# Kernel tuning notes

Hardware: AMD Instinct MI355X
Metric: run time of the kernel (lower is better)

Reference implementation:

```python
import jax, jax.numpy as jnp
import numpy as np

IN_DIM = 128
HID = 128
NUM_CLASSES = 10
N_NODES = 100000
N_EDGES = 1600000
NUM_GRAPHS = 128


def setup_inputs() -> dict:
    key = jax.random.key(0)
    ks = jax.random.split(key, 12)
    X = jax.random.normal(ks[0], (N_NODES, IN_DIM), dtype=jnp.float32)
    EI = jax.random.randint(ks[1], (2, N_EDGES), 0, N_NODES, dtype=jnp.int64)
    batch = jnp.sort(jax.random.randint(ks[2], (N_NODES,), 0, NUM_GRAPHS, dtype=jnp.int64))
    s_in = 1.0 / np.sqrt(IN_DIM)
    s_h = 1.0 / np.sqrt(HID)
    s_m = 1.0 / np.sqrt(2 * HID)
    params = {
        'W1': jax.random.uniform(ks[3], (IN_DIM, HID), jnp.float32, -s_in, s_in),
        'b1': jnp.zeros((HID,), jnp.float32),
        'W2': jax.random.uniform(ks[4], (HID, HID), jnp.float32, -s_h, s_h),
        'b2': jnp.zeros((HID,), jnp.float32),
        'W3': jax.random.uniform(ks[5], (HID, HID), jnp.float32, -s_h, s_h),
        'b3': jnp.zeros((HID,), jnp.float32),
        'Wm1': jax.random.uniform(ks[6], (2 * HID, HID), jnp.float32, -s_m, s_m),
        'bm1': jnp.zeros((HID,), jnp.float32),
        'Wm2': jax.random.uniform(ks[7], (HID, NUM_CLASSES), jnp.float32, -s_h, s_h),
        'bm2': jnp.zeros((NUM_CLASSES,), jnp.float32),
    }
    return dict(X=X, EI=EI, batch=batch, num_graphs=NUM_GRAPHS, **params)


def _gcn_norm(EI, n):
    # add self loops, compute D^{-1/2}[row] * D^{-1/2}[col]
    loops = jnp.arange(n, dtype=EI.dtype)
    row = jnp.concatenate([EI[0], loops])
    col = jnp.concatenate([EI[1], loops])
    deg = jax.ops.segment_sum(jnp.ones_like(row, dtype=jnp.float32), row, num_segments=n)
    dis = (deg + 1e-12) ** -0.5
    norm = dis[row] * dis[col]
    return row, col, norm


def _gcn_layer(x, row, col, norm, W, b):
    h = x @ W + b                       # [N, out]
    msg = h[col] * norm[:, None]        # gather + scale  [E+N, out]
    return jax.ops.segment_sum(msg, row, num_segments=x.shape[0])  # scatter-add


def _pool_mean_max(x, batch, num_graphs):
    s = jax.ops.segment_sum(x, batch, num_segments=num_graphs)
    cnt = jax.ops.segment_sum(jnp.ones((x.shape[0],), x.dtype), batch, num_segments=num_graphs)
    mean = s / (cnt[:, None] + 1e-12)
    mx = jax.ops.segment_max(x, batch, num_segments=num_graphs)
    return jnp.concatenate([mean, mx], axis=1)


def reference(X, EI, batch, num_graphs, W1, b1, W2, b2, W3, b3, Wm1, bm1, Wm2, bm2):
    n = X.shape[0]
    row, col, norm = _gcn_norm(EI, n)
    x = jax.nn.relu(_gcn_layer(X, row, col, norm, W1, b1))
    x = jax.nn.relu(_gcn_layer(x, row, col, norm, W2, b2))
    x = jax.nn.relu(_gcn_layer(x, row, col, norm, W3, b3))
    g = _pool_mean_max(x, batch, num_graphs)
    h = jax.nn.relu(g @ Wm1 + bm1)
    return h @ Wm2 + bm2
```

## Files before the change

kernel.cpp:

```cpp
#include <hip/hip_runtime.h>
#include <hip/hip_fp16.h>
#include <cstdint>
#include <cstddef>

#define DIM 128
#define NG 128
#define NCLS 10
#define PSLICE 8
#define CPAD 64
#define NXCD 8
#define NOWN 32
#define OPX (NOWN / NXCD)
#define NPBLK 1024
#define OCAP 112
#define GRAB 8
#define XCCID_IMM ((31 << 11) | (0 << 6) | 20)

typedef _Float16 f16;
typedef __attribute__((ext_vector_type(8))) _Float16 f16x8;
typedef __attribute__((ext_vector_type(4))) float f32x4;


__global__ __launch_bounds__(256) void k_part(
    const int* __restrict__ rw, const int* __restrict__ cl, int E, int N,
    unsigned long long* __restrict__ buckets, int* __restrict__ bcnt) {
  __shared__ int lcnt[NOWN];
  if (threadIdx.x < NOWN) lcnt[threadIdx.x] = 0;
  __syncthreads();
  int b = blockIdx.x;
  int C = (E + NPBLK - 1) / NPBLK;
  int s = b * C;
  int e = s + C;
  if (e > E) e = E;
  for (int i = s + (int)threadIdx.x; i < e; i += 256) {
    int r = rw[i], c = cl[i];
    int o = (int)(((long long)r * NOWN) / N);
    int sl = atomicAdd(&lcnt[o], 1);
    if (sl < OCAP)
      buckets[((size_t)o * NPBLK + b) * OCAP + sl] =
          ((unsigned long long)(unsigned)r << 32) | (unsigned)c;
  }
  __syncthreads();
  if (threadIdx.x < NOWN) {
    int v = lcnt[threadIdx.x];
    bcnt[threadIdx.x * NPBLK + b] = v < OCAP ? v : OCAP;
  }
}

__global__ __launch_bounds__(256) void k_place(
    const unsigned long long* __restrict__ buckets, const int* __restrict__ bcnt,
    int* __restrict__ cnt, int* __restrict__ csrc, int* __restrict__ work) {
  __shared__ int sg;
  const int ngrab = OPX * NPBLK / GRAB;
  unsigned xcc = __builtin_amdgcn_s_getreg(XCCID_IMM) & (NXCD - 1);
  for (;;) {
    if (threadIdx.x == 0) sg = atomicAdd(&work[xcc], 1);
    __syncthreads();
    int g = sg;
    __syncthreads();
    if (g >= ngrab) break;
    int owner = (int)xcc * OPX + g / (NPBLK / GRAB);
    int blk0 = (g % (NPBLK / GRAB)) * GRAB;
    const int* bc = bcnt + owner * NPBLK + blk0;
    const unsigned long long* bp =
        buckets + ((size_t)owner * NPBLK + blk0) * OCAP;
    for (int j = (int)threadIdx.x; j < GRAB * OCAP; j += 256) {
      int bb = j / OCAP;
      int pos = j % OCAP;
      if (pos < bc[bb]) {
        unsigned long long ent = bp[(size_t)bb * OCAP + pos];
        int r = (int)(unsigned)(ent >> 32);
        int c = (int)(unsigned)(ent & 0xffffffffu);
        int sl = atomicAdd(&cnt[r], 1);
        if (sl < CPAD) csrc[(r << 6) + sl] = c;
      }
    }
  }
}

__global__ void k_dis(const int* __restrict__ cnt, float* __restrict__ dis, int N) {
  int i = blockIdx.x * blockDim.x + threadIdx.x;
  if (i < N) {
    float d = (float)(cnt[i] + 1);
    dis[i] = 1.0f / sqrtf(d);
  }
}

__global__ void k_wt(const float* __restrict__ W1, const float* __restrict__ W2,
                     const float* __restrict__ W3, __half* __restrict__ Wt1,
                     __half* __restrict__ Wt2, __half* __restrict__ Wt3) {
  int gi = blockIdx.x * 256 + threadIdx.x;
  int m = gi / (DIM * DIM);
  int i = gi % (DIM * DIM);
  const float* W = (m == 0) ? W1 : (m == 1) ? W2 : W3;
  __half* Wt = (m == 0) ? Wt1 : (m == 1) ? Wt2 : Wt3;
  int k = i >> 7, c = i & 127;
  Wt[(size_t)c * DIM + k] = __float2half(W[(size_t)k * DIM + c]);
}


template <int FP32IN>
__global__ __launch_bounds__(256, 3) void k_gemm(
    const void* __restrict__ Ain, const __half* __restrict__ Wt,
    const float* __restrict__ bias, const float* __restrict__ dis,
    __half* __restrict__ Hh, int N) {
  int t = threadIdx.x;
  int lane = t & 63;
  int wv = t >> 6;
  int l15 = lane & 15, lg = lane >> 4;
  int cb = (wv & 1) * 64;

  f16x8 bfr[4][4];
#pragma unroll
  for (int ct = 0; ct < 4; ++ct) {
    int c = cb + ct * 16 + l15;
    const f16* wp = (const f16*)Wt + (size_t)c * DIM + lg * 8;
#pragma unroll
    for (int ks = 0; ks < 4; ++ks) bfr[ks][ct] = *(const f16x8*)(wp + ks * 32);
  }
  float bv[4];
#pragma unroll
  for (int ct = 0; ct < 4; ++ct) bv[ct] = bias[cb + ct * 16 + l15];

  const int nt2 = (N + 31) / 32;
  for (int t2 = blockIdx.x; t2 < nt2; t2 += gridDim.x) {
    int row0 = t2 * 32 + (wv >> 1) * 16;
    int rA = row0 + l15;
    if (rA > N - 1) rA = N - 1;
    f16x8 afr[4];
    if constexpr (FP32IN) {
      const float* ap = (const float*)Ain + (size_t)rA * DIM + lg * 8;
#pragma unroll
      for (int ks = 0; ks < 4; ++ks) {
        float4 v0 = *(const float4*)(ap + ks * 32);
        float4 v1 = *(const float4*)(ap + ks * 32 + 4);
        f16x8 a;
        a[0] = (f16)v0.x; a[1] = (f16)v0.y; a[2] = (f16)v0.z; a[3] = (f16)v0.w;
        a[4] = (f16)v1.x; a[5] = (f16)v1.y; a[6] = (f16)v1.z; a[7] = (f16)v1.w;
        afr[ks] = a;
      }
    } else {
      const f16* ap = (const f16*)Ain + (size_t)rA * DIM + lg * 8;
#pragma unroll
      for (int ks = 0; ks < 4; ++ks) afr[ks] = *(const f16x8*)(ap + ks * 32);
    }

    f32x4 acc[4];
#pragma unroll
    for (int ct = 0; ct < 4; ++ct) acc[ct] = (f32x4){0.f, 0.f, 0.f, 0.f};
#pragma unroll
    for (int ks = 0; ks < 4; ++ks)
#pragma unroll
      for (int ct = 0; ct < 4; ++ct)
        acc[ct] = __builtin_amdgcn_mfma_f32_16x16x32_f16(afr[ks], bfr[ks][ct], acc[ct], 0, 0, 0);

#pragma unroll
    for (int j = 0; j < 4; ++j) {
      int r = row0 + lg * 4 + j;
      if (r < N) {
        float dr = dis[r];
#pragma unroll
        for (int ct = 0; ct < 4; ++ct) {
          float o = (acc[ct][j] + bv[ct]) * dr;
          Hh[(size_t)r * DIM + cb + ct * 16 + l15] = __float2half(o);
        }
      }
    }
  }
}


__global__ __launch_bounds__(256) void k_agg(
    const __half* __restrict__ Hh, __half* __restrict__ Ah,
    const int* __restrict__ csrc, const int* __restrict__ cntA,
    const float* __restrict__ dis, int N) {
  int wid = (int)(((size_t)blockIdx.x * blockDim.x + threadIdx.x) >> 6);
  int lane = threadIdx.x & 63;
  if (wid >= N) return;
  int half = lane >> 5;
  int q = lane & 31;
  int cnt = cntA[wid];
  if (cnt > CPAD) cnt = CPAD;
  float dr = dis[wid];
  const int* cp = csrc + ((size_t)wid << 6);
  float4 a0 = {0.f, 0.f, 0.f, 0.f};
  float4 a1 = {0.f, 0.f, 0.f, 0.f};
  float4 a2 = {0.f, 0.f, 0.f, 0.f};
  float4 a3 = {0.f, 0.f, 0.f, 0.f};
  int i = half;
  for (; i + 6 < cnt; i += 8) {
    int c0 = cp[i], c1 = cp[i + 2], c2 = cp[i + 4], c3 = cp[i + 6];
    uint2 u0 = *(const uint2*)(Hh + (size_t)c0 * DIM + q * 4);
    uint2 u1 = *(const uint2*)(Hh + (size_t)c1 * DIM + q * 4);
    uint2 u2 = *(const uint2*)(Hh + (size_t)c2 * DIM + q * 4);
    uint2 u3 = *(const uint2*)(Hh + (size_t)c3 * DIM + q * 4);
    float2 f;
    f = __half22float2(*reinterpret_cast<__half2*>(&u0.x)); a0.x += f.x; a0.y += f.y;
    f = __half22float2(*reinterpret_cast<__half2*>(&u0.y)); a0.z += f.x; a0.w += f.y;
    f = __half22float2(*reinterpret_cast<__half2*>(&u1.x)); a1.x += f.x; a1.y += f.y;
    f = __half22float2(*reinterpret_cast<__half2*>(&u1.y)); a1.z += f.x; a1.w += f.y;
    f = __half22float2(*reinterpret_cast<__half2*>(&u2.x)); a2.x += f.x; a2.y += f.y;
    f = __half22float2(*reinterpret_cast<__half2*>(&u2.y)); a2.z += f.x; a2.w += f.y;
    f = __half22float2(*reinterpret_cast<__half2*>(&u3.x)); a3.x += f.x; a3.y += f.y;
    f = __half22float2(*reinterpret_cast<__half2*>(&u3.y)); a3.z += f.x; a3.w += f.y;
  }
  for (; i < cnt; i += 2) {
    int c0 = cp[i];
    uint2 u0 = *(const uint2*)(Hh + (size_t)c0 * DIM + q * 4);
    float2 f;
    f = __half22float2(*reinterpret_cast<__half2*>(&u0.x)); a0.x += f.x; a0.y += f.y;
    f = __half22float2(*reinterpret_cast<__half2*>(&u0.y)); a0.z += f.x; a0.w += f.y;
  }
  float ax = (a0.x + a1.x) + (a2.x + a3.x);
  float ay = (a0.y + a1.y) + (a2.y + a3.y);
  float az = (a0.z + a1.z) + (a2.z + a3.z);
  float aw = (a0.w + a1.w) + (a2.w + a3.w);
  ax += __shfl_xor(ax, 32);
  ay += __shfl_xor(ay, 32);
  az += __shfl_xor(az, 32);
  aw += __shfl_xor(aw, 32);
  if (lane < 32) {
    uint2 us = *(const uint2*)(Hh + (size_t)wid * DIM + q * 4);
    float2 s0 = __half22float2(*reinterpret_cast<__half2*>(&us.x));
    float2 s1 = __half22float2(*reinterpret_cast<__half2*>(&us.y));
    float ox = fmaxf(dr * (ax + s0.x), 0.f);
    float oy = fmaxf(dr * (ay + s0.y), 0.f);
    float oz = fmaxf(dr * (az + s1.x), 0.f);
    float ow = fmaxf(dr * (aw + s1.y), 0.f);
    __half2 p0 = __floats2half2_rn(ox, oy);
    __half2 p1 = __floats2half2_rn(oz, ow);
    uint2 u;
    u.x = *(unsigned int*)&p0;
    u.y = *(unsigned int*)&p1;
    *(uint2*)(Ah + (size_t)wid * DIM + q * 4) = u;
  }
}


__global__ void k_bounds(const int* __restrict__ batch, int N, int G,
                         int* __restrict__ starts) {
  int i = blockIdx.x * blockDim.x + threadIdx.x;
  if (i >= N) return;
  int b = batch[i];
  int pb = (i == 0) ? -1 : batch[i - 1];
  for (int g = pb + 1; g <= b; ++g) starts[g] = i;
  if (i == N - 1) {
    for (int g = b + 1; g <= G; ++g) starts[g] = N;
  }
}

__global__ void k_pool1(const __half* __restrict__ A, const int* __restrict__ starts,
                        float* __restrict__ part) {
  int g = blockIdx.x / PSLICE, sl = blockIdx.x % PSLICE;
  int c = threadIdx.x;
  int s = starts[g], e = starts[g + 1];
  int len = e - s;
  int ns = s + (len * sl) / PSLICE;
  int ne = s + (len * (sl + 1)) / PSLICE;
  float sum = 0.f, mx = -INFINITY;
  for (int n = ns; n < ne; ++n) {
    float v = __half2float(A[(size_t)n * DIM + c]);
    sum += v;
    mx = fmaxf(mx, v);
  }
  part[((size_t)(g * PSLICE + sl) * 2 + 0) * DIM + c] = sum;
  part[((size_t)(g * PSLICE + sl) * 2 + 1) * DIM + c] = mx;
}

__global__ void k_pool2(const float* __restrict__ part, const int* __restrict__ starts,
                        float* __restrict__ GF) {
  int g = blockIdx.x;
  int c = threadIdx.x;
  float sum = 0.f, mx = -INFINITY;
  for (int sl = 0; sl < PSLICE; ++sl) {
    sum += part[((size_t)(g * PSLICE + sl) * 2 + 0) * DIM + c];
    mx = fmaxf(mx, part[((size_t)(g * PSLICE + sl) * 2 + 1) * DIM + c]);
  }
  int cntg = starts[g + 1] - starts[g];
  GF[(size_t)g * 256 + c] = sum / ((float)cntg + 1e-12f);
  GF[(size_t)g * 256 + 128 + c] = mx;
}


__global__ void k_mlp1(const float* __restrict__ GF, const float* __restrict__ Wm1,
                       const float* __restrict__ bm1, float* __restrict__ H1) {
  __shared__ float gs[256];
  int g = blockIdx.x, j = threadIdx.x;
  gs[j] = GF[(size_t)g * 256 + j];
  gs[j + 128] = GF[(size_t)g * 256 + 128 + j];
  __syncthreads();
  float acc = bm1[j];
#pragma unroll 8
  for (int k = 0; k < 256; ++k) acc = fmaf(gs[k], Wm1[k * DIM + j], acc);
  H1[(size_t)g * DIM + j] = fmaxf(acc, 0.f);
}

__global__ void k_mlp2(const float* __restrict__ H1, const float* __restrict__ Wm2,
                       const float* __restrict__ bm2, float* __restrict__ out) {
  __shared__ float hs[DIM];
  int g = blockIdx.x, j = threadIdx.x;
  hs[j] = H1[(size_t)g * DIM + j];
  hs[j + 64] = H1[(size_t)g * DIM + j + 64];
  __syncthreads();
  if (j < NCLS) {
    float acc = bm2[j];
#pragma unroll 8
    for (int k = 0; k < DIM; ++k) acc = fmaf(hs[k], Wm2[k * NCLS + j], acc);
    out[(size_t)g * NCLS + j] = acc;
  }
}


static inline size_t al256(size_t x) { return (x + 255) & ~(size_t)255; }

extern "C" void kernel_launch(void* const* d_in, const int* in_sizes, int n_in,
                              void* d_out, int out_size, void* d_ws, size_t ws_size,
                              hipStream_t stream) {
  const float* X = (const float*)d_in[0];
  const int* EI = (const int*)d_in[1];
  const int* batch = (const int*)d_in[2];
  const float* W1 = (const float*)d_in[4];
  const float* b1 = (const float*)d_in[5];
  const float* W2 = (const float*)d_in[6];
  const float* b2 = (const float*)d_in[7];
  const float* W3 = (const float*)d_in[8];
  const float* b3 = (const float*)d_in[9];
  const float* Wm1 = (const float*)d_in[10];
  const float* bm1 = (const float*)d_in[11];
  const float* Wm2 = (const float*)d_in[12];
  const float* bm2 = (const float*)d_in[13];
  float* OUT = (float*)d_out;

  const int N = in_sizes[0] / DIM;
  const int E = in_sizes[1] / 2;
  const int G = NG;

  const int* EI_row = EI;
  const int* EI_col = EI + E;

  char* p = (char*)d_ws;
  size_t off = 0;
  auto take = [&](size_t bytes) { void* r = p + off; off = al256(off + bytes); return r; };

  int* cnt = (int*)take((size_t)N * 4);
  int* work = (int*)take((size_t)NXCD * 4);
  int* bcnt = (int*)take((size_t)NOWN * NPBLK * 4);
  int* starts = (int*)take((size_t)(G + 1) * 4);
  float* dis = (float*)take((size_t)N * 4);
  int* csrc = (int*)take((size_t)N * CPAD * 4);
  unsigned long long* buckets =
      (unsigned long long*)take((size_t)NOWN * NPBLK * OCAP * 8);
  __half* Hh = (__half*)take((size_t)N * DIM * 2);
  __half* Ah = (__half*)take((size_t)N * DIM * 2);
  __half* Wt1 = (__half*)take((size_t)DIM * DIM * 2);
  __half* Wt2 = (__half*)take((size_t)DIM * DIM * 2);
  __half* Wt3 = (__half*)take((size_t)DIM * DIM * 2);
  float* part = (float*)take((size_t)G * PSLICE * 2 * DIM * 4);
  float* GF = (float*)take((size_t)G * 256 * 4);
  float* H1 = (float*)take((size_t)G * DIM * 4);
  (void)ws_size; (void)n_in; (void)out_size;

  hipMemsetAsync(cnt, 0, (size_t)N * 4, stream);
  hipMemsetAsync(work, 0, (size_t)NXCD * 4, stream);

  k_part<<<NPBLK, 256, 0, stream>>>(EI_row, EI_col, E, N, buckets, bcnt);
  k_place<<<1024, 256, 0, stream>>>(buckets, bcnt, cnt, csrc, work);
  k_dis<<<(N + 255) / 256, 256, 0, stream>>>(cnt, dis, N);
  k_wt<<<192, 256, 0, stream>>>(W1, W2, W3, Wt1, Wt2, Wt3);

  const int aggBlocks = (int)(((size_t)N * 64 + 255) / 256);

  k_gemm<1><<<512, 256, 0, stream>>>(X, Wt1, b1, dis, Hh, N);
  k_agg<<<aggBlocks, 256, 0, stream>>>(Hh, Ah, csrc, cnt, dis, N);
  k_gemm<0><<<512, 256, 0, stream>>>(Ah, Wt2, b2, dis, Hh, N);
  k_agg<<<aggBlocks, 256, 0, stream>>>(Hh, Ah, csrc, cnt, dis, N);
  k_gemm<0><<<512, 256, 0, stream>>>(Ah, Wt3, b3, dis, Hh, N);
  k_agg<<<aggBlocks, 256, 0, stream>>>(Hh, Ah, csrc, cnt, dis, N);

  k_bounds<<<(N + 255) / 256, 256, 0, stream>>>(batch, N, G, starts);
  k_pool1<<<G * PSLICE, DIM, 0, stream>>>(Ah, starts, part);
  k_pool2<<<G, DIM, 0, stream>>>(part, starts, GF);

  k_mlp1<<<G, DIM, 0, stream>>>(GF, Wm1, bm1, H1);
  k_mlp2<<<G, 64, 0, stream>>>(H1, Wm2, bm2, OUT);
}
```

Measured before the change: 440.1 us.

## Build CSR per row-range in LDS with small buckets and overflow list

Edges are now partitioned into 256 fixed row ranges of 391 rows, each with small per-block buckets of 16 slots; edges beyond a bucket's capacity go to a global overflow list. Each placement block builds its own range's padded adjacency and degree counts with LDS atomics, then writes them out with coalesced 16-byte stores. This replaces scattered global atomics on the per-node count array, the XCD-aware work-stealing loop and the count memset. The trade-offs are about 100 KB of LDS per placement block, a scan of the whole overflow list by every block, and a fixed rows-per-range constant that only covers N up to 100096.

```diff
diff --git a/kernel.cpp b/kernel.cpp
--- a/kernel.cpp
+++ b/kernel.cpp
@@ -8,13 +8,11 @@
 #define NCLS 10
 #define PSLICE 8
 #define CPAD 64
-#define NXCD 8
-#define NOWN 32
-#define OPX (NOWN / NXCD)
+#define NOWN 256
+#define RPB 391
 #define NPBLK 1024
-#define OCAP 112
-#define GRAB 8
-#define XCCID_IMM ((31 << 11) | (0 << 6) | 20)
+#define OCAP 16
+#define OVCAP 65536
 
 typedef _Float16 f16;
 typedef __attribute__((ext_vector_type(8))) _Float16 f16x8;
@@ -22,8 +20,9 @@
 
 
 __global__ __launch_bounds__(256) void k_part(
-    const int* __restrict__ rw, const int* __restrict__ cl, int E, int N,
-    unsigned long long* __restrict__ buckets, int* __restrict__ bcnt) {
+    const int* __restrict__ rw, const int* __restrict__ cl, int E,
+    unsigned long long* __restrict__ buckets, int* __restrict__ bcnt,
+    unsigned long long* __restrict__ ovf, int* __restrict__ ovfn) {
   __shared__ int lcnt[NOWN];
   if (threadIdx.x < NOWN) lcnt[threadIdx.x] = 0;
   __syncthreads();
@@ -34,11 +33,16 @@
   if (e > E) e = E;
   for (int i = s + (int)threadIdx.x; i < e; i += 256) {
     int r = rw[i], c = cl[i];
-    int o = (int)(((long long)r * NOWN) / N);
+    unsigned long long ent =
+        ((unsigned long long)(unsigned)r << 32) | (unsigned)c;
+    int o = (unsigned)r / RPB;
     int sl = atomicAdd(&lcnt[o], 1);
-    if (sl < OCAP)
-      buckets[((size_t)o * NPBLK + b) * OCAP + sl] =
-          ((unsigned long long)(unsigned)r << 32) | (unsigned)c;
+    if (sl < OCAP) {
+      buckets[((size_t)o * NPBLK + b) * OCAP + sl] = ent;
+    } else {
+      int oi = atomicAdd(ovfn, 1);
+      if (oi < OVCAP) ovf[oi] = ent;
+    }
   }
   __syncthreads();
   if (threadIdx.x < NOWN) {
@@ -49,33 +53,50 @@
 
 __global__ __launch_bounds__(256) void k_place(
     const unsigned long long* __restrict__ buckets, const int* __restrict__ bcnt,
-    int* __restrict__ cnt, int* __restrict__ csrc, int* __restrict__ work) {
-  __shared__ int sg;
-  const int ngrab = OPX * NPBLK / GRAB;
-  unsigned xcc = __builtin_amdgcn_s_getreg(XCCID_IMM) & (NXCD - 1);
-  for (;;) {
-    if (threadIdx.x == 0) sg = atomicAdd(&work[xcc], 1);
-    __syncthreads();
-    int g = sg;
-    __syncthreads();
-    if (g >= ngrab) break;
-    int owner = (int)xcc * OPX + g / (NPBLK / GRAB);
-    int blk0 = (g % (NPBLK / GRAB)) * GRAB;
-    const int* bc = bcnt + owner * NPBLK + blk0;
-    const unsigned long long* bp =
-        buckets + ((size_t)owner * NPBLK + blk0) * OCAP;
-    for (int j = (int)threadIdx.x; j < GRAB * OCAP; j += 256) {
-      int bb = j / OCAP;
-      int pos = j % OCAP;
-      if (pos < bc[bb]) {
-        unsigned long long ent = bp[(size_t)bb * OCAP + pos];
-        int r = (int)(unsigned)(ent >> 32);
-        int c = (int)(unsigned)(ent & 0xffffffffu);
-        int sl = atomicAdd(&cnt[r], 1);
-        if (sl < CPAD) csrc[(r << 6) + sl] = c;
-      }
+    const unsigned long long* __restrict__ ovf, const int* __restrict__ ovfn,
+    int* __restrict__ cnt, int* __restrict__ csrc, int N) {
+  extern __shared__ int sm[];
+  int* lcnt = sm;
+  int* csr = sm + ((RPB + 3) & ~3);
+  int o = blockIdx.x;
+  int r0 = o * RPB;
+  int rows = N - r0;
+  if (rows > RPB) rows = RPB;
+  if (rows <= 0) return;
+  for (int i = threadIdx.x; i < rows; i += 256) lcnt[i] = 0;
+  __syncthreads();
+  const int* bc = bcnt + o * NPBLK;
+  const unsigned long long* bp = buckets + (size_t)o * NPBLK * OCAP;
+  for (int j = (int)threadIdx.x; j < NPBLK * OCAP; j += 256) {
+    int seg = j >> 4;
+    int pos = j & 15;
+    if (pos < bc[seg]) {
+      unsigned long long ent = bp[j];
+      int r = (int)(unsigned)(ent >> 32);
+      int c = (int)(unsigned)(ent & 0xffffffffu);
+      int li = r - r0;
+      int sl = atomicAdd(&lcnt[li], 1);
+      if (sl < CPAD) csr[(li << 6) + sl] = c;
     }
   }
+  int nov = *ovfn;
+  if (nov > OVCAP) nov = OVCAP;
+  for (int j = (int)threadIdx.x; j < nov; j += 256) {
+    unsigned long long ent = ovf[j];
+    int r = (int)(unsigned)(ent >> 32);
+    int li = r - r0;
+    if (li >= 0 && li < rows) {
+      int c = (int)(unsigned)(ent & 0xffffffffu);
+      int sl = atomicAdd(&lcnt[li], 1);
+      if (sl < CPAD) csr[(li << 6) + sl] = c;
+    }
+  }
+  __syncthreads();
+  uint4* dst = (uint4*)(csrc + ((size_t)r0 << 6));
+  const uint4* src = (const uint4*)csr;
+  int n4 = rows * 16;
+  for (int j = (int)threadIdx.x; j < n4; j += 256) dst[j] = src[j];
+  for (int i = threadIdx.x; i < rows; i += 256) cnt[r0 + i] = lcnt[i];
 }
 
 __global__ void k_dis(const int* __restrict__ cnt, float* __restrict__ dis, int N) {
@@ -343,8 +364,9 @@
   auto take = [&](size_t bytes) { void* r = p + off; off = al256(off + bytes); return r; };
 
   int* cnt = (int*)take((size_t)N * 4);
-  int* work = (int*)take((size_t)NXCD * 4);
   int* bcnt = (int*)take((size_t)NOWN * NPBLK * 4);
+  int* ovfn = (int*)take(256);
+  unsigned long long* ovf = (unsigned long long*)take((size_t)OVCAP * 8);
   int* starts = (int*)take((size_t)(G + 1) * 4);
   float* dis = (float*)take((size_t)N * 4);
   int* csrc = (int*)take((size_t)N * CPAD * 4);
@@ -360,11 +382,11 @@
   float* H1 = (float*)take((size_t)G * DIM * 4);
   (void)ws_size; (void)n_in; (void)out_size;
 
-  hipMemsetAsync(cnt, 0, (size_t)N * 4, stream);
-  hipMemsetAsync(work, 0, (size_t)NXCD * 4, stream);
-
-  k_part<<<NPBLK, 256, 0, stream>>>(EI_row, EI_col, E, N, buckets, bcnt);
-  k_place<<<1024, 256, 0, stream>>>(buckets, bcnt, cnt, csrc, work);
+  hipMemsetAsync(ovfn, 0, 4, stream);
+
+  k_part<<<NPBLK, 256, 0, stream>>>(EI_row, EI_col, E, buckets, bcnt, ovf, ovfn);
+  const int placeLds = ((RPB + 3) & ~3) * 4 + RPB * 64 * 4;
+  k_place<<<NOWN, 256, placeLds, stream>>>(buckets, bcnt, ovf, ovfn, cnt, csrc, N);
   k_dis<<<(N + 255) / 256, 256, 0, stream>>>(cnt, dis, N);
   k_wt<<<192, 256, 0, stream>>>(W1, W2, W3, Wt1, Wt2, Wt3);
 
```

Measured after the change: 383.4 us. 1.15x faster.
